# Optimization experiments

Hardware: AMD Instinct MI355X
Metric: run time of the kernel (lower is better)

Reference implementation:

```python
import jax, jax.numpy as jnp
import numpy as np

H = 64
EPS = 1e-8


def _quat_mul(q1, q2):
    w1, x1, y1, z1 = q1[..., 0], q1[..., 1], q1[..., 2], q1[..., 3]
    w2, x2, y2, z2 = q2[..., 0], q2[..., 1], q2[..., 2], q2[..., 3]
    return jnp.stack([
        w1 * w2 - x1 * x2 - y1 * y2 - z1 * z2,
        w1 * x2 + x1 * w2 + y1 * z2 - z1 * y2,
        w1 * y2 - x1 * z2 + y1 * w2 + z1 * x2,
        w1 * z2 + x1 * y2 - y1 * x2 + z1 * w2,
    ], axis=-1)


def _quat_conj(q):
    return q * jnp.array([1.0, -1.0, -1.0, -1.0], dtype=q.dtype)


def _oct_mul(o1, o2):
    # Cayley-Dickson: (a,b)(c,d) = (ac - conj(d) b, d a + b conj(c))
    a, b = o1[..., :4], o1[..., 4:]
    c, d = o2[..., :4], o2[..., 4:]
    re = _quat_mul(a, c) - _quat_mul(_quat_conj(d), b)
    im = _quat_mul(d, a) + _quat_mul(b, _quat_conj(c))
    return jnp.concatenate([re, im], axis=-1)


def setup_inputs() -> dict:
    key = jax.random.key(0)
    k0, k1, k2, k3, k4 = jax.random.split(key, 5)
    B, N, D = 16, 4096, H * 8
    o = jax.random.normal(k0, (B, N, D), dtype=jnp.float32)
    # scalar_mlp: Linear(2,32) -> GELU -> Linear(32,3), torch layout (out, in)
    W1 = jax.random.normal(k1, (32, 2), dtype=jnp.float32) * (1.0 / np.sqrt(2.0))
    b1 = jax.random.normal(k2, (32,), dtype=jnp.float32) * 0.01
    W2 = jax.random.normal(k3, (3, 32), dtype=jnp.float32) * (1.0 / np.sqrt(32.0))
    b2 = jax.random.normal(k4, (3,), dtype=jnp.float32) * 0.01
    alpha = jnp.asarray(0.25, dtype=jnp.float32)
    return {"o": o, "W1": W1, "b1": b1, "W2": W2, "b2": b2, "alpha": alpha}


def reference(o, W1, b1, W2, b2, alpha):
    B, N, D = o.shape
    oh = o.reshape(B, N, H, 8)                       # [B,N,H,8]
    r = oh[..., 0]                                   # real part [B,N,H]
    n = jnp.linalg.norm(oh[..., 1:], axis=-1)        # ||imag|| [B,N,H]
    inv = jnp.stack([r, n], axis=-1)                 # [B,N,H,2]
    h = jax.nn.gelu(inv @ W1.T + b1, approximate=False)
    scalars = h @ W2.T + b2                          # [B,N,H,3]
    a, b, c = scalars[..., 0], scalars[..., 1], scalars[..., 2]
    o2 = _oct_mul(oh, oh)
    o3 = _oct_mul(oh, o2)
    upd = a[..., None] * oh + b[..., None] * o2 + c[..., None] * o3
    upd = upd / jnp.maximum(jnp.linalg.norm(upd, axis=-1, keepdims=True), EPS)
    upd = upd.reshape(B, N, D)
    lam = jax.nn.sigmoid(alpha)
    return (1.0 - lam) * o + lam * upd
```

## Files before the change

### kernel.cpp

```cpp
#include <hip/hip_runtime.h>
#include <math.h>


__global__ __launch_bounds__(256) void g2_ffn_kernel(
    const float* __restrict__ o,
    const float* __restrict__ W1,
    const float* __restrict__ b1,
    const float* __restrict__ W2,
    const float* __restrict__ b2,
    const float* __restrict__ alpha_p,
    float* __restrict__ out,
    int half)
{
    int i = blockIdx.x * blockDim.x + threadIdx.x;
    if (i >= half) return;
    size_t i0 = (size_t)i;
    size_t i1 = i0 + (size_t)half;

    const float4* ip = (const float4*)o;
    float4 A0 = ip[2 * i0], A1 = ip[2 * i0 + 1];
    float4 B0 = ip[2 * i1], B1 = ip[2 * i1 + 1];

    float wa = A0.x;
    float na2 = A0.y * A0.y;
    na2 = fmaf(A0.z, A0.z, na2);  na2 = fmaf(A0.w, A0.w, na2);
    na2 = fmaf(A1.x, A1.x, na2);  na2 = fmaf(A1.y, A1.y, na2);
    na2 = fmaf(A1.z, A1.z, na2);  na2 = fmaf(A1.w, A1.w, na2);
    float nna = __builtin_amdgcn_sqrtf(na2);
    float sa  = fmaf(wa, wa, na2);

    float wb = B0.x;
    float nb2 = B0.y * B0.y;
    nb2 = fmaf(B0.z, B0.z, nb2);  nb2 = fmaf(B0.w, B0.w, nb2);
    nb2 = fmaf(B1.x, B1.x, nb2);  nb2 = fmaf(B1.y, B1.y, nb2);
    nb2 = fmaf(B1.z, B1.z, nb2);  nb2 = fmaf(B1.w, B1.w, nb2);
    float nnb = __builtin_amdgcn_sqrtf(nb2);
    float sb  = fmaf(wb, wb, nb2);

    const float C_  = 0.84932180f;
    const float K1_ = 0.2727375f;
    const float KF_ = 0.5887050f;

    float aA = 0.0f, aB = 0.0f, aC = 0.0f;
    float bA = 0.0f, bB = 0.0f, bC = 0.0f;

#pragma unroll
    for (int j = 0; j < 32; ++j) {
        float wr  = W1[2 * j];
        float wn  = W1[2 * j + 1];
        float bj  = b1[j];
        float w2a = W2[j];
        float w2b = W2[32 + j];
        float w2c = W2[64 + j];

        float xa = C_ * fmaf(wr, wa, fmaf(wn, nna, bj));
        float xb = C_ * fmaf(wr, wb, fmaf(wn, nnb, bj));

        float ea = __builtin_amdgcn_exp2f(-(xa * xa));
        float eb = __builtin_amdgcn_exp2f(-(xb * xb));

        float ta = __builtin_amdgcn_rcpf(fmaf(K1_, fabsf(xa), 1.0f));
        float tb = __builtin_amdgcn_rcpf(fmaf(K1_, fabsf(xb), 1.0f));

        float pa = fmaf(1.061405429f, ta, -1.453152027f);
        float pb = fmaf(1.061405429f, tb, -1.453152027f);
        pa = fmaf(pa, ta, 1.421413741f);   pb = fmaf(pb, tb, 1.421413741f);
        pa = fmaf(pa, ta, -0.284496736f);  pb = fmaf(pb, tb, -0.284496736f);
        pa = fmaf(pa, ta, 0.254829592f);   pb = fmaf(pb, tb, 0.254829592f);

        float ga = fmaf(fabsf(xa), fmaf(-(pa * ta), ea, 1.0f), xa);
        float gb = fmaf(fabsf(xb), fmaf(-(pb * tb), eb, 1.0f), xb);

        aA = fmaf(w2a, ga, aA);   bA = fmaf(w2a, gb, bA);
        aB = fmaf(w2b, ga, aB);   bB = fmaf(w2b, gb, bB);
        aC = fmaf(w2c, ga, aC);   bC = fmaf(w2c, gb, bC);
    }

    float avA = fmaf(KF_, aA, b2[0]);
    float bvA = fmaf(KF_, aB, b2[1]);
    float cvA = fmaf(KF_, aC, b2[2]);
    float avB = fmaf(KF_, bA, b2[0]);
    float bvB = fmaf(KF_, bB, b2[1]);
    float cvB = fmaf(KF_, bC, b2[2]);

    float alpha_in = alpha_p[0];
    float lam = __builtin_amdgcn_rcpf(
        1.0f + __builtin_amdgcn_exp2f(-alpha_in * 1.44269504f));
    float oml = 1.0f - lam;

    float qa  = fmaf(4.0f * wa, wa, -sa);
    float ala = fmaf(cvA, qa, fmaf(bvA + bvA, wa, avA));
    float bea = -(sa * fmaf(cvA + cvA, wa, bvA));
    float t2a = fmaf(ala * bea, wa + wa, fmaf(ala * ala, sa, bea * bea));
    float inva = __builtin_amdgcn_rsqf(fmaxf(t2a, 1e-16f));
    float laa = lam * ala * inva;
    float lba = lam * bea * inva;
    float sca = oml + laa;

    float4 ra0, ra1;
    ra0.x = fmaf(sca, A0.x, lba);
    ra0.y = sca * A0.y;  ra0.z = sca * A0.z;  ra0.w = sca * A0.w;
    ra1.x = sca * A1.x;  ra1.y = sca * A1.y;  ra1.z = sca * A1.z;  ra1.w = sca * A1.w;

    float qb  = fmaf(4.0f * wb, wb, -sb);
    float alb = fmaf(cvB, qb, fmaf(bvB + bvB, wb, avB));
    float beb = -(sb * fmaf(cvB + cvB, wb, bvB));
    float t2b = fmaf(alb * beb, wb + wb, fmaf(alb * alb, sb, beb * beb));
    float invb = __builtin_amdgcn_rsqf(fmaxf(t2b, 1e-16f));
    float lab = lam * alb * invb;
    float lbb = lam * beb * invb;
    float scb = oml + lab;

    float4 rb0, rb1;
    rb0.x = fmaf(scb, B0.x, lbb);
    rb0.y = scb * B0.y;  rb0.z = scb * B0.z;  rb0.w = scb * B0.w;
    rb1.x = scb * B1.x;  rb1.y = scb * B1.y;  rb1.z = scb * B1.z;  rb1.w = scb * B1.w;

    float4* op = (float4*)out;
    op[2 * i0]     = ra0;
    op[2 * i0 + 1] = ra1;
    op[2 * i1]     = rb0;
    op[2 * i1 + 1] = rb1;
}

extern "C" void kernel_launch(void* const* d_in, const int* in_sizes, int n_in,
                              void* d_out, int out_size, void* d_ws, size_t ws_size,
                              hipStream_t stream) {
    const float* o     = (const float*)d_in[0];
    const float* W1    = (const float*)d_in[1];
    const float* b1    = (const float*)d_in[2];
    const float* W2    = (const float*)d_in[3];
    const float* b2    = (const float*)d_in[4];
    const float* alpha = (const float*)d_in[5];
    float* out = (float*)d_out;

    int n_oct = in_sizes[0] / 8;
    int half = n_oct >> 1;
    int block = 256;
    int grid = (half + block - 1) / block;
    g2_ffn_kernel<<<grid, block, 0, stream>>>(o, W1, b1, W2, b2, alpha, out, half);
}
```

Before: 247.8 us.

## Replace erf-based GELU with shared-memory cubic Hermite lookup table

Builds a 256-entry cubic Hermite table of GELU over [-6.4, 6.4] in LDS per block, then evaluates GELU via a clamp, floor, LDS gather and a cubic polynomial instead of exp2, rcp and a degree-5 polynomial. The aim is to cut transcendental and VALU work in the 32-iteration hidden loop. In exchange each block pays for table construction plus a __syncthreads, and the loop now does random-index LDS loads that can hit bank conflicts. Accuracy depends on table resolution, and very negative inputs are clamped to the first entry.

```diff
diff --git a/kernel.cpp b/kernel.cpp
--- a/kernel.cpp
+++ b/kernel.cpp
@@ -1,6 +1,24 @@
 #include <hip/hip_runtime.h>
 #include <math.h>
 
+#define NTAB     256
+#define TAB_LO   -6.4f
+#define TAB_H    0.05f
+#define TAB_INVH 20.0f
+#define TAB_BIAS 128.0f
+
+__device__ __forceinline__ float fast_erf(float x) {
+    float z = fabsf(x);
+    float t = __builtin_amdgcn_rcpf(fmaf(0.3275911f, z, 1.0f));
+    float p = fmaf(1.061405429f, t, -1.453152027f);
+    p = fmaf(p, t, 1.421413741f);
+    p = fmaf(p, t, -0.284496736f);
+    p = fmaf(p, t, 0.254829592f);
+    p = p * t;
+    float e = __builtin_amdgcn_exp2f(-(z * z) * 1.44269504f);
+    float r = fmaf(-p, e, 1.0f);
+    return copysignf(r, x);
+}
 
 __global__ __launch_bounds__(256) void g2_ffn_kernel(
     const float* __restrict__ o,
@@ -12,7 +30,31 @@
     float* __restrict__ out,
     int half)
 {
-    int i = blockIdx.x * blockDim.x + threadIdx.x;
+    __shared__ float4 tab[NTAB];
+
+    int tid = threadIdx.x;
+
+    {
+        float m0 = fmaf((float)tid, TAB_H, TAB_LO);
+        float m1 = m0 + TAB_H;
+        float Phi0 = 0.5f * (1.0f + fast_erf(m0 * 0.70710678f));
+        float Phi1 = 0.5f * (1.0f + fast_erf(m1 * 0.70710678f));
+        float phi0 = 0.39894228f * __builtin_amdgcn_exp2f(-(m0 * m0) * 0.72134752f);
+        float phi1 = 0.39894228f * __builtin_amdgcn_exp2f(-(m1 * m1) * 0.72134752f);
+        float g0 = m0 * Phi0;
+        float g1 = m1 * Phi1;
+        float d0 = TAB_H * fmaf(m0, phi0, Phi0);
+        float d1 = TAB_H * fmaf(m1, phi1, Phi1);
+        float4 c;
+        c.x = g0;
+        c.y = d0;
+        c.z = 3.0f * (g1 - g0) - 2.0f * d0 - d1;
+        c.w = 2.0f * (g0 - g1) + d0 + d1;
+        tab[tid] = c;
+    }
+    __syncthreads();
+
+    int i = blockIdx.x * blockDim.x + tid;
     if (i >= half) return;
     size_t i0 = (size_t)i;
     size_t i1 = i0 + (size_t)half;
@@ -37,10 +79,6 @@
     float nnb = __builtin_amdgcn_sqrtf(nb2);
     float sb  = fmaf(wb, wb, nb2);
 
-    const float C_  = 0.84932180f;
-    const float K1_ = 0.2727375f;
-    const float KF_ = 0.5887050f;
-
     float aA = 0.0f, aB = 0.0f, aC = 0.0f;
     float bA = 0.0f, bB = 0.0f, bC = 0.0f;
 
@@ -53,35 +91,34 @@
         float w2b = W2[32 + j];
         float w2c = W2[64 + j];
 
-        float xa = C_ * fmaf(wr, wa, fmaf(wn, nna, bj));
-        float xb = C_ * fmaf(wr, wb, fmaf(wn, nnb, bj));
+        float pa = fmaf(wr, wa, fmaf(wn, nna, bj));
+        float pb = fmaf(wr, wb, fmaf(wn, nnb, bj));
 
-        float ea = __builtin_amdgcn_exp2f(-(xa * xa));
-        float eb = __builtin_amdgcn_exp2f(-(xb * xb));
+        float ua = fminf(fmaxf(fmaf(pa, TAB_INVH, TAB_BIAS), 0.0f), 255.0f);
+        float ub = fminf(fmaxf(fmaf(pb, TAB_INVH, TAB_BIAS), 0.0f), 255.0f);
+        float fia = floorf(ua);
+        float fib = floorf(ub);
+        float fa = ua - fia;
+        float fb = ub - fib;
+        float4 ca = tab[(int)fia];
+        float4 cb = tab[(int)fib];
 
-        float ta = __builtin_amdgcn_rcpf(fmaf(K1_, fabsf(xa), 1.0f));
-        float tb = __builtin_amdgcn_rcpf(fmaf(K1_, fabsf(xb), 1.0f));
-
-        float pa = fmaf(1.061405429f, ta, -1.453152027f);
-        float pb = fmaf(1.061405429f, tb, -1.453152027f);
-        pa = fmaf(pa, ta, 1.421413741f);   pb = fmaf(pb, tb, 1.421413741f);
-        pa = fmaf(pa, ta, -0.284496736f);  pb = fmaf(pb, tb, -0.284496736f);
-        pa = fmaf(pa, ta, 0.254829592f);   pb = fmaf(pb, tb, 0.254829592f);
-
-        float ga = fmaf(fabsf(xa), fmaf(-(pa * ta), ea, 1.0f), xa);
-        float gb = fmaf(fabsf(xb), fmaf(-(pb * tb), eb, 1.0f), xb);
+        float ga = fmaf(fmaf(fmaf(ca.w, fa, ca.z), fa, ca.y), fa, ca.x);
+        float gb = fmaf(fmaf(fmaf(cb.w, fb, cb.z), fb, cb.y), fb, cb.x);
+        ga = (pa >= 6.34f) ? pa : ga;
+        gb = (pb >= 6.34f) ? pb : gb;
 
         aA = fmaf(w2a, ga, aA);   bA = fmaf(w2a, gb, bA);
         aB = fmaf(w2b, ga, aB);   bB = fmaf(w2b, gb, bB);
         aC = fmaf(w2c, ga, aC);   bC = fmaf(w2c, gb, bC);
     }
 
-    float avA = fmaf(KF_, aA, b2[0]);
-    float bvA = fmaf(KF_, aB, b2[1]);
-    float cvA = fmaf(KF_, aC, b2[2]);
-    float avB = fmaf(KF_, bA, b2[0]);
-    float bvB = fmaf(KF_, bB, b2[1]);
-    float cvB = fmaf(KF_, bC, b2[2]);
+    float avA = aA + b2[0];
+    float bvA = aB + b2[1];
+    float cvA = aC + b2[2];
+    float avB = bA + b2[0];
+    float bvB = bB + b2[1];
+    float cvB = bC + b2[2];
 
     float alpha_in = alpha_p[0];
     float lam = __builtin_amdgcn_rcpf(
```

Result: no change. 246.0 us (-0.8%).
